# Kernel optimization log

Measured on AMD Instinct MI355X. Metric: run time of the kernel, lower is better.

## Reference

```python
import jax, jax.numpy as jnp
import numpy as np

EMB = 1024
DM = 64
NH = 16

def setup_inputs() -> dict:
    key = jax.random.key(0)
    ks = jax.random.split(key, 11)
    bs, slen = 2, 2048
    s = 1.0 / np.sqrt(EMB)
    inp = {
        'Q': jax.random.normal(ks[0], (bs, slen, EMB), jnp.float32),
        'K': jax.random.normal(ks[1], (bs, slen, EMB), jnp.float32),
        'V': jax.random.normal(ks[2], (bs, slen, EMB), jnp.float32),
        'Wq': jax.random.normal(ks[3], (EMB, DM * NH), jnp.float32) * s,
        'bq': jnp.zeros((DM * NH,), jnp.float32),
        'Wk': jax.random.normal(ks[4], (EMB, DM * NH), jnp.float32) * s,
        'bk': jnp.zeros((DM * NH,), jnp.float32),
        'Wv': jax.random.normal(ks[5], (EMB, DM * NH), jnp.float32) * s,
        'bv': jnp.zeros((DM * NH,), jnp.float32),
        'Wo': jax.random.normal(ks[6], (DM * NH, EMB), jnp.float32) * (1.0 / np.sqrt(DM * NH)),
        'bo': jnp.zeros((EMB,), jnp.float32),
    }
    return inp

def reference(Q, K, V, Wq, bq, Wk, bk, Wv, bv, Wo, bo):
    bs, q_len, _ = Q.shape
    kv_len = K.shape[1]
    scale = 1.0 / np.sqrt(DM)
    # project and split heads: (n, l, h, d)
    q = (scale * (Q @ Wq + bq)).reshape(bs, q_len, NH, DM)
    k = (K @ Wk + bk).reshape(bs, kv_len, NH, DM)
    v = (V @ Wv + bv).reshape(bs, kv_len, NH, DM)
    # scores (n, h, l, s) -- full S x S matrix, as in the original
    qk = jnp.einsum('nlhd,nshd->nhls', q, k)
    a = jax.nn.softmax(qk, axis=-1)  # dropout p=0 -> identity
    o = jnp.einsum('nhls,nshd->nlhd', a, v).reshape(bs, q_len, NH * DM)
    return o @ Wo + bo
```

## Files before the change

### kernel.cpp

```cpp
#include <hip/hip_runtime.h>
#include <cstdint>
#include <cstddef>

#define EMB  1024
#define DM   64
#define NH   16
#define SLEN 2048
#define BS   2

typedef _Float16 f16x8 __attribute__((ext_vector_type(8)));
typedef _Float16 f16x4 __attribute__((ext_vector_type(4)));
typedef __fp16   hf2   __attribute__((ext_vector_type(2)));
typedef __fp16   hf4   __attribute__((ext_vector_type(4)));
typedef __fp16   hf8   __attribute__((ext_vector_type(8)));
typedef float    f32x4 __attribute__((ext_vector_type(4)));

#define ASYNC_LD16(gp, lp)                                                        \
    __builtin_amdgcn_global_load_lds(                                             \
        (const __attribute__((address_space(1))) void*)(gp),                      \
        (__attribute__((address_space(3))) void*)(lp), 16, 0, 0)

__global__ __launch_bounds__(256)
void prep(const float* __restrict__ Q, const float* __restrict__ K,
          const float* __restrict__ V,
          const float* __restrict__ Wq, const float* __restrict__ Wk,
          const float* __restrict__ Wv, const float* __restrict__ Wo,
          _Float16* __restrict__ Qh, _Float16* __restrict__ Kh,
          _Float16* __restrict__ Vh,
          _Float16* __restrict__ WqT, _Float16* __restrict__ WkT,
          _Float16* __restrict__ WvT, _Float16* __restrict__ WoT)
{
    __shared__ float t[64][65];
    const int z = blockIdx.z;
    if (z < 3) {
        const float* in  = (z == 0) ? Q : (z == 1) ? K : V;
        _Float16*    out = (z == 0) ? Qh : (z == 1) ? Kh : Vh;
        size_t i = ((size_t)blockIdx.x * 256 + threadIdx.x) * 8;
        float4 a = *(const float4*)(in + i);
        float4 b = *(const float4*)(in + i + 4);
        f16x8 o;
        o[0] = (_Float16)a.x; o[1] = (_Float16)a.y; o[2] = (_Float16)a.z; o[3] = (_Float16)a.w;
        o[4] = (_Float16)b.x; o[5] = (_Float16)b.y; o[6] = (_Float16)b.z; o[7] = (_Float16)b.w;
        *(f16x8*)(out + i) = o;
        return;
    }
    if (blockIdx.x >= 256) return;
    const float* W;
    _Float16*    T;
    switch (z - 3) {
        case 0:  W = Wq; T = WqT; break;
        case 1:  W = Wk; T = WkT; break;
        case 2:  W = Wv; T = WvT; break;
        default: W = Wo; T = WoT; break;
    }
    const int tid = threadIdx.x;
    const int bn  = (blockIdx.x & 15) * 64;
    const int bk  = (blockIdx.x >> 4) * 64;

    #pragma unroll
    for (int p = 0; p < 4; ++p) {
        int row = p * 16 + (tid >> 4);
        int col = (tid & 15) * 4;
        float4 v = *(const float4*)(W + (size_t)(bk + row) * EMB + bn + col);
        t[row][col+0] = v.x; t[row][col+1] = v.y; t[row][col+2] = v.z; t[row][col+3] = v.w;
    }
    __syncthreads();
    #pragma unroll
    for (int p = 0; p < 4; ++p) {
        int nr = p * 16 + (tid >> 4);
        int kc = (tid & 15) * 4;
        f16x4 o;
        o[0] = (_Float16)t[kc+0][nr];
        o[1] = (_Float16)t[kc+1][nr];
        o[2] = (_Float16)t[kc+2][nr];
        o[3] = (_Float16)t[kc+3][nr];
        *(f16x4*)&T[(size_t)(bn + nr) * EMB + bk + kc] = o;
    }
}

__device__ __forceinline__
void gemm_core(const _Float16* __restrict__ A, const _Float16* __restrict__ Bt,
               const float* __restrict__ bias, float* __restrict__ Cf,
               _Float16* __restrict__ Ch, int M, int N, int K,
               float scale, int mode, int bx, int by)
{
    __shared__ __align__(16) _Float16 As[2][128 * 32];
    __shared__ __align__(16) _Float16 Bs[2][128 * 32];

    const int tid  = threadIdx.x;
    const int lane = tid & 63;
    const int wave = tid >> 6;
    const int c    = lane & 15;
    const int quad = lane >> 4;
    const int bm   = by * 128;
    const int bn   = bx * 128;
    const int wm   = (wave >> 1) * 64;
    const int wn   = (wave & 1) * 64;

    f32x4 acc[4][4];
    #pragma unroll
    for (int i = 0; i < 4; ++i)
        #pragma unroll
        for (int j = 0; j < 4; ++j)
            #pragma unroll
            for (int r = 0; r < 4; ++r) acc[i][j][r] = 0.f;

    const size_t Kb = (size_t)K * 2;
    const int    lc = ((tid & 3) ^ ((tid >> 4) & 3)) * 16;
    const char* gA = (const char*)A  + (size_t)(bm + (tid >> 2)) * Kb + lc;
    const char* gB = (const char*)Bt + (size_t)(bn + (tid >> 2)) * Kb + lc;

    const int NS = K / 32;

    auto stage = [&](int buf, int t) {
        const size_t ko = (size_t)t * 64;
        char* lA = (char*)&As[buf][0] + wave * 1024;
        char* lB = (char*)&Bs[buf][0] + wave * 1024;
        ASYNC_LD16(gA + ko,           lA);
        ASYNC_LD16(gA + 64*Kb + ko,   lA + 4096);
        ASYNC_LD16(gB + ko,           lB);
        ASYNC_LD16(gB + 64*Kb + ko,   lB + 4096);
    };

    stage(0, 0);
    __syncthreads();

    int cur = 0;
    for (int t = 0; t < NS; ++t) {
        if (t + 1 < NS) stage(cur ^ 1, t + 1);

        f16x8 af[4], bf[4];
        #pragma unroll
        for (int i = 0; i < 4; ++i)
            af[i] = *(const f16x8*)
                &As[cur][(wm + i*16 + c) * 32 + ((quad ^ ((c >> 2) & 3)) * 8)];
        #pragma unroll
        for (int j = 0; j < 4; ++j)
            bf[j] = *(const f16x8*)
                &Bs[cur][(wn + j*16 + c) * 32 + ((quad ^ ((c >> 2) & 3)) * 8)];
        #pragma unroll
        for (int i = 0; i < 4; ++i)
            #pragma unroll
            for (int j = 0; j < 4; ++j)
                acc[i][j] = __builtin_amdgcn_mfma_f32_16x16x32_f16(af[i], bf[j], acc[i][j], 0, 0, 0);

        __syncthreads();
        cur ^= 1;
    }

    float bcol[4];
    #pragma unroll
    for (int j = 0; j < 4; ++j) bcol[j] = bias[bn + wn + j * 16 + c];

    #pragma unroll
    for (int i = 0; i < 4; ++i) {
        int m0 = bm + wm + i * 16 + quad * 4;
        #pragma unroll
        for (int j = 0; j < 4; ++j) {
            int n = bn + wn + j * 16 + c;
            if (mode == 0) {
                #pragma unroll
                for (int r = 0; r < 4; ++r)
                    Cf[(size_t)(m0 + r) * N + n] = acc[i][j][r] + bcol[j];
            } else if (mode == 1) {
                int h = n >> 6, d = n & 63;
                #pragma unroll
                for (int r = 0; r < 4; ++r) {
                    int mm = m0 + r;
                    int b = mm >> 11, l = mm & (SLEN - 1);
                    Ch[(((size_t)(b * NH + h)) * SLEN + l) * DM + d] =
                        (_Float16)((acc[i][j][r] + bcol[j]) * scale);
                }
            } else {
                int h = n >> 6, d = n & 63;
                int b = m0 >> 11, l = m0 & (SLEN - 1);
                f16x4 o;
                #pragma unroll
                for (int r = 0; r < 4; ++r)
                    o[r] = (_Float16)(acc[i][j][r] + bcol[j]);
                *(f16x4*)&Ch[(((size_t)(b * NH + h)) * DM + d) * SLEN + l] = o;
            }
        }
    }
}

__device__ __forceinline__ void xcd_swz(int& bx, int& by)
{
    int wid = blockIdx.x + 8 * blockIdx.y;
    bx = wid >> 5;
    by = wid & 31;
}

__global__ __launch_bounds__(256)
void gemm_qkv(const _Float16* __restrict__ Qh, const _Float16* __restrict__ Kh,
              const _Float16* __restrict__ Vh,
              const _Float16* __restrict__ WqT, const _Float16* __restrict__ WkT,
              const _Float16* __restrict__ WvT,
              const float* __restrict__ bq, const float* __restrict__ bk,
              const float* __restrict__ bv,
              _Float16* __restrict__ q_ws, _Float16* __restrict__ k_ws,
              _Float16* __restrict__ v_ws)
{
    const _Float16 *A, *Bt;
    const float* bias;
    _Float16* Ch;
    float scale;
    int mode;
    if (blockIdx.z == 0)      { A = Qh; Bt = WqT; bias = bq; Ch = q_ws; scale = 0.18033688f; mode = 1; }
    else if (blockIdx.z == 1) { A = Kh; Bt = WkT; bias = bk; Ch = k_ws; scale = 1.0f;        mode = 1; }
    else                      { A = Vh; Bt = WvT; bias = bv; Ch = v_ws; scale = 1.0f;        mode = 2; }
    int bx, by; xcd_swz(bx, by);
    gemm_core(A, Bt, bias, nullptr, Ch, BS * SLEN, NH * DM, EMB, scale, mode, bx, by);
}

__global__ __launch_bounds__(256)
void gemm_out(const _Float16* __restrict__ Oh, const _Float16* __restrict__ WoT,
              const float* __restrict__ bo, float* __restrict__ out)
{
    int bx, by; xcd_swz(bx, by);
    gemm_core(Oh, WoT, bo, out, nullptr, BS * SLEN, EMB, NH * DM, 1.0f, 0, bx, by);
}

__global__ __launch_bounds__(512)
void attn_mfma(const _Float16* __restrict__ qw, const _Float16* __restrict__ kw,
               const _Float16* __restrict__ vwT, _Float16* __restrict__ ow)
{
    __shared__ __align__(16) _Float16 Kt[4][64 * 64];
    __shared__ __align__(16) _Float16 Vt[4][64 * 64];

    const int tid  = threadIdx.x;
    const int lane = tid & 63;
    const int wave = tid >> 6;
    const int c    = lane & 15;
    const int quad = lane >> 4;
    const int qg   = wave & 3;
    const int kh   = wave >> 2;
    const int bh   = blockIdx.y;
    const int b    = bh >> 4;
    const int h    = bh & 15;
    const int qbase = blockIdx.x * 128 + qg * 32;

    const _Float16* kb = kw  + (size_t)bh * SLEN * DM;
    const _Float16* vb = vwT + (size_t)bh * DM * SLEN;
    const _Float16* qb = qw  + (size_t)bh * SLEN * DM;

    f16x8 qf[2][2];
    #pragma unroll
    for (int t = 0; t < 2; ++t)
        #pragma unroll
        for (int ch = 0; ch < 2; ++ch)
            qf[t][ch] = *(const f16x8*)(qb + (size_t)(qbase + t*16 + c) * DM + ch*32 + quad*8);

    f32x4 oacc[2][4];
    f32x4 lacc[2];
    #pragma unroll
    for (int t = 0; t < 2; ++t) {
        #pragma unroll
        for (int dg = 0; dg < 4; ++dg)
            #pragma unroll
            for (int r = 0; r < 4; ++r) oacc[t][dg][r] = 0.f;
        #pragma unroll
        for (int r = 0; r < 4; ++r) lacc[t][r] = 0.f;
    }

    const f16x8 ones8 = {(_Float16)1.f, (_Float16)1.f, (_Float16)1.f, (_Float16)1.f,
                         (_Float16)1.f, (_Float16)1.f, (_Float16)1.f, (_Float16)1.f};
    const f32x4 zero4 = {0.f, 0.f, 0.f, 0.f};

    const int r0  = wave * 8 + (lane >> 3);
    const int lc0 = (((lane & 7) ^ ((lane >> 3) & 7)) * 16);
    const char* gk = (const char*)kb + r0 * 128 + lc0;
    const char* gv = (const char*)vb + (size_t)r0 * 4096 + lc0;

    auto stage = [&](int buf) {
        char* pk = (char*)&Kt[buf][0] + wave * 1024;
        char* pv = (char*)&Vt[buf][0] + wave * 1024;
        ASYNC_LD16(gk, pk);
        ASYNC_LD16(gv, pv);
        gk += 8192;
        gv += 128;
    };

    stage(0); stage(1); stage(2);
    asm volatile("s_waitcnt vmcnt(4)" ::: "memory");
    __builtin_amdgcn_s_barrier();
    asm volatile("" ::: "memory");

    const int NT = SLEN / 64;
    for (int t = 0; t < NT; ++t) {
        stage((t + 3) & 3);
        const int cb = t & 3;

        f16x8 kf[2][2];
        #pragma unroll
        for (int kg = 0; kg < 2; ++kg)
            #pragma unroll
            for (int ch = 0; ch < 2; ++ch)
                kf[kg][ch] = *(const f16x8*)
                    &Kt[cb][(kh*32 + kg*16 + c) * 64 + (((ch*4 + quad) ^ (c & 7)) * 8)];

        f32x4 s[2][2];
        #pragma unroll
        for (int t2 = 0; t2 < 2; ++t2)
            #pragma unroll
            for (int kg = 0; kg < 2; ++kg) {
                s[t2][kg] = __builtin_amdgcn_mfma_f32_16x16x32_f16(kf[kg][0], qf[t2][0], zero4,    0, 0, 0);
                s[t2][kg] = __builtin_amdgcn_mfma_f32_16x16x32_f16(kf[kg][1], qf[t2][1], s[t2][kg], 0, 0, 0);
            }

        f16x8 pf8[2];
        #pragma unroll
        for (int t2 = 0; t2 < 2; ++t2) {
            hf4 h4[2];
            #pragma unroll
            for (int u = 0; u < 2; ++u) {
                float p0 = __builtin_amdgcn_exp2f(s[t2][u][0]);
                float p1 = __builtin_amdgcn_exp2f(s[t2][u][1]);
                float p2 = __builtin_amdgcn_exp2f(s[t2][u][2]);
                float p3 = __builtin_amdgcn_exp2f(s[t2][u][3]);
                hf2 lo = __builtin_amdgcn_cvt_pkrtz(p0, p1);
                hf2 hi = __builtin_amdgcn_cvt_pkrtz(p2, p3);
                h4[u] = __builtin_shufflevector(lo, hi, 0, 1, 2, 3);
            }
            hf8 h8 = __builtin_shufflevector(h4[0], h4[1], 0, 1, 2, 3, 4, 5, 6, 7);
            pf8[t2] = __builtin_bit_cast(f16x8, h8);
        }

        #pragma unroll
        for (int t2 = 0; t2 < 2; ++t2)
            lacc[t2] = __builtin_amdgcn_mfma_f32_16x16x32_f16(pf8[t2], ones8, lacc[t2], 0, 0, 0);

        #pragma unroll
        for (int dg = 0; dg < 4; ++dg) {
            f16x4 vf[2];
            #pragma unroll
            for (int u = 0; u < 2; ++u)
                vf[u] = *(const f16x4*)
                    &Vt[cb][(dg*16 + c) * 64 +
                            (((kh*4 + 2*u + (quad >> 1)) ^ (c & 7)) * 8) + (quad & 1) * 4];
            f16x8 v8 = __builtin_shufflevector(vf[0], vf[1], 0, 1, 2, 3, 4, 5, 6, 7);
            #pragma unroll
            for (int t2 = 0; t2 < 2; ++t2)
                oacc[t2][dg] = __builtin_amdgcn_mfma_f32_16x16x32_f16(pf8[t2], v8, oacc[t2][dg], 0, 0, 0);
        }

        asm volatile("s_waitcnt vmcnt(4)" ::: "memory");
        __builtin_amdgcn_s_barrier();
        asm volatile("" ::: "memory");
    }

    __syncthreads();

    float* mb = (float*)&Kt[0][0];
    #pragma unroll
    for (int t = 0; t < 2; ++t) {
        if (kh == 1) {
            float* p = mb + ((qg * 64 + lane) * 20);
            *(f32x4*)(p +  0) = oacc[t][0];
            *(f32x4*)(p +  4) = oacc[t][1];
            *(f32x4*)(p +  8) = oacc[t][2];
            *(f32x4*)(p + 12) = oacc[t][3];
            *(f32x4*)(p + 16) = lacc[t];
        }
        __syncthreads();
        if (kh == 0) {
            const float* p = mb + ((qg * 64 + lane) * 20);
            f32x4 po[4], pl;
            po[0] = *(const f32x4*)(p +  0);
            po[1] = *(const f32x4*)(p +  4);
            po[2] = *(const f32x4*)(p +  8);
            po[3] = *(const f32x4*)(p + 12);
            pl    = *(const f32x4*)(p + 16);
            #pragma unroll
            for (int r = 0; r < 4; ++r) {
                float linv = 1.0f / (lacc[t][r] + pl[r]);
                int row = qbase + t*16 + quad*4 + r;
                #pragma unroll
                for (int dg = 0; dg < 4; ++dg)
                    ow[((size_t)b * SLEN + row) * EMB + h * DM + dg*16 + c] =
                        (_Float16)((oacc[t][dg][r] + po[dg][r]) * linv);
            }
        }
        __syncthreads();
    }
}

extern "C" void kernel_launch(void* const* d_in, const int* in_sizes, int n_in,
                              void* d_out, int out_size, void* d_ws, size_t ws_size,
                              hipStream_t stream)
{
    const float* Q  = (const float*)d_in[0];
    const float* K  = (const float*)d_in[1];
    const float* V  = (const float*)d_in[2];
    const float* Wq = (const float*)d_in[3];
    const float* bq = (const float*)d_in[4];
    const float* Wk = (const float*)d_in[5];
    const float* bk = (const float*)d_in[6];
    const float* Wv = (const float*)d_in[7];
    const float* bv = (const float*)d_in[8];
    const float* Wo = (const float*)d_in[9];
    const float* bo = (const float*)d_in[10];
    float* out = (float*)d_out;

    const size_t MN = (size_t)BS * SLEN * NH * DM;
    const size_t WW = (size_t)EMB * NH * DM;

    _Float16* base = (_Float16*)d_ws;
    _Float16* Qh   = base;
    _Float16* Kh   = Qh  + MN;
    _Float16* Vh   = Kh  + MN;
    _Float16* WqT  = Vh  + MN;
    _Float16* WkT  = WqT + WW;
    _Float16* WvT  = WkT + WW;
    _Float16* WoT  = WvT + WW;
    _Float16* q_ws = WoT + WW;
    _Float16* k_ws = q_ws + MN;
    _Float16* v_ws = k_ws + MN;
    _Float16* o_ws = v_ws + MN;

    dim3 blk(256);

    prep<<<dim3(2048, 1, 7), blk, 0, stream>>>(Q, K, V, Wq, Wk, Wv, Wo,
                                               Qh, Kh, Vh, WqT, WkT, WvT, WoT);

    gemm_qkv<<<dim3(8, 32, 3), blk, 0, stream>>>(Qh, Kh, Vh, WqT, WkT, WvT,
                                                 bq, bk, bv, q_ws, k_ws, v_ws);

    attn_mfma<<<dim3(SLEN / 128, BS * NH), dim3(512), 0, stream>>>(q_ws, k_ws, v_ws, o_ws);

    gemm_out<<<dim3(8, 32, 1), blk, 0, stream>>>(o_ws, WoT, bo, out);
}
```

Before: 229.6 us.

## Fuse fp32-to-fp16 activation conversion into QKV GEMM and retile GEMMs

Removes the separate pass that converts Q, K and V activations from fp32 to fp16. The QKV GEMM now loads fp32 A tiles through registers, converts them and writes them into swizzled LDS, while B still uses async global-to-LDS loads. GEMM tiles change from 128x128x32 to 64x128x64, doubling the grid. This saves a full read/write round trip of the activations, but the A path is now synchronous register loads and reads twice the bytes per element.

```diff
diff --git a/kernel.cpp b/kernel.cpp
--- a/kernel.cpp
+++ b/kernel.cpp
@@ -21,33 +21,15 @@
         (__attribute__((address_space(3))) void*)(lp), 16, 0, 0)
 
 __global__ __launch_bounds__(256)
-void prep(const float* __restrict__ Q, const float* __restrict__ K,
-          const float* __restrict__ V,
-          const float* __restrict__ Wq, const float* __restrict__ Wk,
+void prep(const float* __restrict__ Wq, const float* __restrict__ Wk,
           const float* __restrict__ Wv, const float* __restrict__ Wo,
-          _Float16* __restrict__ Qh, _Float16* __restrict__ Kh,
-          _Float16* __restrict__ Vh,
           _Float16* __restrict__ WqT, _Float16* __restrict__ WkT,
           _Float16* __restrict__ WvT, _Float16* __restrict__ WoT)
 {
     __shared__ float t[64][65];
-    const int z = blockIdx.z;
-    if (z < 3) {
-        const float* in  = (z == 0) ? Q : (z == 1) ? K : V;
-        _Float16*    out = (z == 0) ? Qh : (z == 1) ? Kh : Vh;
-        size_t i = ((size_t)blockIdx.x * 256 + threadIdx.x) * 8;
-        float4 a = *(const float4*)(in + i);
-        float4 b = *(const float4*)(in + i + 4);
-        f16x8 o;
-        o[0] = (_Float16)a.x; o[1] = (_Float16)a.y; o[2] = (_Float16)a.z; o[3] = (_Float16)a.w;
-        o[4] = (_Float16)b.x; o[5] = (_Float16)b.y; o[6] = (_Float16)b.z; o[7] = (_Float16)b.w;
-        *(f16x8*)(out + i) = o;
-        return;
-    }
-    if (blockIdx.x >= 256) return;
     const float* W;
     _Float16*    T;
-    switch (z - 3) {
+    switch (blockIdx.z) {
         case 0:  W = Wq; T = WqT; break;
         case 1:  W = Wk; T = WkT; break;
         case 2:  W = Wv; T = WvT; break;
@@ -78,72 +60,133 @@
     }
 }
 
+template <bool A32>
 __device__ __forceinline__
-void gemm_core(const _Float16* __restrict__ A, const _Float16* __restrict__ Bt,
+void gemm_core(const void* __restrict__ Aptr, const _Float16* __restrict__ Bt,
                const float* __restrict__ bias, float* __restrict__ Cf,
                _Float16* __restrict__ Ch, int M, int N, int K,
                float scale, int mode, int bx, int by)
 {
-    __shared__ __align__(16) _Float16 As[2][128 * 32];
-    __shared__ __align__(16) _Float16 Bs[2][128 * 32];
+    __shared__ __align__(16) _Float16 As[2][64 * 64];
+    __shared__ __align__(16) _Float16 Bs[2][128 * 64];
 
     const int tid  = threadIdx.x;
     const int lane = tid & 63;
     const int wave = tid >> 6;
     const int c    = lane & 15;
     const int quad = lane >> 4;
-    const int bm   = by * 128;
+    const int bm   = by * 64;
     const int bn   = bx * 128;
-    const int wm   = (wave >> 1) * 64;
+    const int wm   = (wave >> 1) * 32;
     const int wn   = (wave & 1) * 64;
 
-    f32x4 acc[4][4];
-    #pragma unroll
-    for (int i = 0; i < 4; ++i)
+    f32x4 acc[2][4];
+    #pragma unroll
+    for (int i = 0; i < 2; ++i)
         #pragma unroll
         for (int j = 0; j < 4; ++j)
             #pragma unroll
             for (int r = 0; r < 4; ++r) acc[i][j][r] = 0.f;
 
     const size_t Kb = (size_t)K * 2;
-    const int    lc = ((tid & 3) ^ ((tid >> 4) & 3)) * 16;
-    const char* gA = (const char*)A  + (size_t)(bm + (tid >> 2)) * Kb + lc;
-    const char* gB = (const char*)Bt + (size_t)(bn + (tid >> 2)) * Kb + lc;
-
-    const int NS = K / 32;
-
-    auto stage = [&](int buf, int t) {
-        const size_t ko = (size_t)t * 64;
+    const int    lc = ((tid & 7) ^ ((tid >> 3) & 7)) * 16;
+    const char* gB = (const char*)Bt + (size_t)(bn + (tid >> 3)) * Kb + lc;
+
+    const char*  gA16 = nullptr;
+    const float* gA32 = nullptr;
+    int aswz0 = 0, aswz1 = 0;
+    if constexpr (A32) {
+        const int ar  = tid >> 2;
+        const int acg = tid & 3;
+        gA32  = (const float*)Aptr + (size_t)(bm + ar) * K + acg * 16;
+        aswz0 = ar * 64 + (((2*acg    ) ^ (ar & 7)) * 8);
+        aswz1 = ar * 64 + (((2*acg + 1) ^ (ar & 7)) * 8);
+    } else {
+        gA16 = (const char*)Aptr + (size_t)(bm + (tid >> 3)) * Kb + lc;
+    }
+
+    const int NS = K / 64;
+
+    auto stageB = [&](int buf, int t) {
+        const size_t ko = (size_t)t * 128;
+        char* lB = (char*)&Bs[buf][0] + wave * 1024;
+        ASYNC_LD16(gB + ko,           lB);
+        ASYNC_LD16(gB + 32*Kb + ko,   lB + 4096);
+        ASYNC_LD16(gB + 64*Kb + ko,   lB + 8192);
+        ASYNC_LD16(gB + 96*Kb + ko,   lB + 12288);
+    };
+    auto stageA16 = [&](int buf, int t) {
+        const size_t ko = (size_t)t * 128;
         char* lA = (char*)&As[buf][0] + wave * 1024;
-        char* lB = (char*)&Bs[buf][0] + wave * 1024;
-        ASYNC_LD16(gA + ko,           lA);
-        ASYNC_LD16(gA + 64*Kb + ko,   lA + 4096);
-        ASYNC_LD16(gB + ko,           lB);
-        ASYNC_LD16(gB + 64*Kb + ko,   lB + 4096);
+        ASYNC_LD16(gA16 + ko,         lA);
+        ASYNC_LD16(gA16 + 32*Kb + ko, lA + 4096);
     };
-
-    stage(0, 0);
+    auto writeA32 = [&](int buf, const float4& a0, const float4& a1,
+                        const float4& a2, const float4& a3) {
+        f16x8 h0, h1;
+        h0[0] = (_Float16)a0.x; h0[1] = (_Float16)a0.y;
+        h0[2] = (_Float16)a0.z; h0[3] = (_Float16)a0.w;
+        h0[4] = (_Float16)a1.x; h0[5] = (_Float16)a1.y;
+        h0[6] = (_Float16)a1.z; h0[7] = (_Float16)a1.w;
+        h1[0] = (_Float16)a2.x; h1[1] = (_Float16)a2.y;
+        h1[2] = (_Float16)a2.z; h1[3] = (_Float16)a2.w;
+        h1[4] = (_Float16)a3.x; h1[5] = (_Float16)a3.y;
+        h1[6] = (_Float16)a3.z; h1[7] = (_Float16)a3.w;
+        *(f16x8*)&As[buf][aswz0] = h0;
+        *(f16x8*)&As[buf][aswz1] = h1;
+    };
+
+    if constexpr (A32) {
+        float4 a0 = *(const float4*)(gA32 + 0);
+        float4 a1 = *(const float4*)(gA32 + 4);
+        float4 a2 = *(const float4*)(gA32 + 8);
+        float4 a3 = *(const float4*)(gA32 + 12);
+        stageB(0, 0);
+        writeA32(0, a0, a1, a2, a3);
+    } else {
+        stageA16(0, 0);
+        stageB(0, 0);
+    }
     __syncthreads();
 
     int cur = 0;
     for (int t = 0; t < NS; ++t) {
-        if (t + 1 < NS) stage(cur ^ 1, t + 1);
-
-        f16x8 af[4], bf[4];
-        #pragma unroll
-        for (int i = 0; i < 4; ++i)
-            af[i] = *(const f16x8*)
-                &As[cur][(wm + i*16 + c) * 32 + ((quad ^ ((c >> 2) & 3)) * 8)];
-        #pragma unroll
-        for (int j = 0; j < 4; ++j)
-            bf[j] = *(const f16x8*)
-                &Bs[cur][(wn + j*16 + c) * 32 + ((quad ^ ((c >> 2) & 3)) * 8)];
-        #pragma unroll
-        for (int i = 0; i < 4; ++i)
+        float4 a0, a1, a2, a3;
+        if constexpr (A32) {
+            if (t + 1 < NS) {
+                const float* p = gA32 + (size_t)(t + 1) * 64;
+                a0 = *(const float4*)(p + 0);
+                a1 = *(const float4*)(p + 4);
+                a2 = *(const float4*)(p + 8);
+                a3 = *(const float4*)(p + 12);
+            }
+        }
+        if (t + 1 < NS) {
+            if constexpr (!A32) stageA16(cur ^ 1, t + 1);
+            stageB(cur ^ 1, t + 1);
+        }
+
+        #pragma unroll
+        for (int kk = 0; kk < 2; ++kk) {
+            f16x8 af[2], bf[4];
+            #pragma unroll
+            for (int i = 0; i < 2; ++i)
+                af[i] = *(const f16x8*)
+                    &As[cur][(wm + i*16 + c) * 64 + (((kk*4 + quad) ^ (c & 7)) * 8)];
             #pragma unroll
             for (int j = 0; j < 4; ++j)
-                acc[i][j] = __builtin_amdgcn_mfma_f32_16x16x32_f16(af[i], bf[j], acc[i][j], 0, 0, 0);
-
+                bf[j] = *(const f16x8*)
+                    &Bs[cur][(wn + j*16 + c) * 64 + (((kk*4 + quad) ^ (c & 7)) * 8)];
+            #pragma unroll
+            for (int i = 0; i < 2; ++i)
+                #pragma unroll
+                for (int j = 0; j < 4; ++j)
+                    acc[i][j] = __builtin_amdgcn_mfma_f32_16x16x32_f16(af[i], bf[j], acc[i][j], 0, 0, 0);
+        }
+
+        if constexpr (A32) {
+            if (t + 1 < NS) writeA32(cur ^ 1, a0, a1, a2, a3);
+        }
         __syncthreads();
         cur ^= 1;
     }
@@ -153,7 +196,7 @@
     for (int j = 0; j < 4; ++j) bcol[j] = bias[bn + wn + j * 16 + c];
 
     #pragma unroll
-    for (int i = 0; i < 4; ++i) {
+    for (int i = 0; i < 2; ++i) {
         int m0 = bm + wm + i * 16 + quad * 4;
         #pragma unroll
         for (int j = 0; j < 4; ++j) {
@@ -187,13 +230,13 @@
 __device__ __forceinline__ void xcd_swz(int& bx, int& by)
 {
     int wid = blockIdx.x + 8 * blockIdx.y;
-    bx = wid >> 5;
-    by = wid & 31;
+    bx = wid >> 6;
+    by = wid & 63;
 }
 
 __global__ __launch_bounds__(256)
-void gemm_qkv(const _Float16* __restrict__ Qh, const _Float16* __restrict__ Kh,
-              const _Float16* __restrict__ Vh,
+void gemm_qkv(const float* __restrict__ Q, const float* __restrict__ K,
+              const float* __restrict__ V,
               const _Float16* __restrict__ WqT, const _Float16* __restrict__ WkT,
               const _Float16* __restrict__ WvT,
               const float* __restrict__ bq, const float* __restrict__ bk,
@@ -201,16 +244,17 @@
               _Float16* __restrict__ q_ws, _Float16* __restrict__ k_ws,
               _Float16* __restrict__ v_ws)
 {
-    const _Float16 *A, *Bt;
+    const float* A;
+    const _Float16* Bt;
     const float* bias;
     _Float16* Ch;
     float scale;
     int mode;
-    if (blockIdx.z == 0)      { A = Qh; Bt = WqT; bias = bq; Ch = q_ws; scale = 0.18033688f; mode = 1; }
-    else if (blockIdx.z == 1) { A = Kh; Bt = WkT; bias = bk; Ch = k_ws; scale = 1.0f;        mode = 1; }
-    else                      { A = Vh; Bt = WvT; bias = bv; Ch = v_ws; scale = 1.0f;        mode = 2; }
+    if (blockIdx.z == 0)      { A = Q; Bt = WqT; bias = bq; Ch = q_ws; scale = 0.18033688f; mode = 1; }
+    else if (blockIdx.z == 1) { A = K; Bt = WkT; bias = bk; Ch = k_ws; scale = 1.0f;        mode = 1; }
+    else                      { A = V; Bt = WvT; bias = bv; Ch = v_ws; scale = 1.0f;        mode = 2; }
     int bx, by; xcd_swz(bx, by);
-    gemm_core(A, Bt, bias, nullptr, Ch, BS * SLEN, NH * DM, EMB, scale, mode, bx, by);
+    gemm_core<true>(A, Bt, bias, nullptr, Ch, BS * SLEN, NH * DM, EMB, scale, mode, bx, by);
 }
 
 __global__ __launch_bounds__(256)
@@ -218,7 +262,7 @@
               const float* __restrict__ bo, float* __restrict__ out)
 {
     int bx, by; xcd_swz(bx, by);
-    gemm_core(Oh, WoT, bo, out, nullptr, BS * SLEN, EMB, NH * DM, 1.0f, 0, bx, by);
+    gemm_core<false>(Oh, WoT, bo, out, nullptr, BS * SLEN, EMB, NH * DM, 1.0f, 0, bx, by);
 }
 
 __global__ __launch_bounds__(512)
@@ -304,7 +348,7 @@
         for (int t2 = 0; t2 < 2; ++t2)
             #pragma unroll
             for (int kg = 0; kg < 2; ++kg) {
-                s[t2][kg] = __builtin_amdgcn_mfma_f32_16x16x32_f16(kf[kg][0], qf[t2][0], zero4,    0, 0, 0);
+                s[t2][kg] = __builtin_amdgcn_mfma_f32_16x16x32_f16(kf[kg][0], qf[t2][0], zero4,     0, 0, 0);
                 s[t2][kg] = __builtin_amdgcn_mfma_f32_16x16x32_f16(kf[kg][1], qf[t2][1], s[t2][kg], 0, 0, 0);
             }
 
@@ -406,10 +450,7 @@
     const size_t WW = (size_t)EMB * NH * DM;
 
     _Float16* base = (_Float16*)d_ws;
-    _Float16* Qh   = base;
-    _Float16* Kh   = Qh  + MN;
-    _Float16* Vh   = Kh  + MN;
-    _Float16* WqT  = Vh  + MN;
+    _Float16* WqT  = base;
     _Float16* WkT  = WqT + WW;
     _Float16* WvT  = WkT + WW;
     _Float16* WoT  = WvT + WW;
@@ -420,13 +461,13 @@
 
     dim3 blk(256);
 
-    prep<<<dim3(2048, 1, 7), blk, 0, stream>>>(Q, K, V, Wq, Wk, Wv, Wo,
-                                               Qh, Kh, Vh, WqT, WkT, WvT, WoT);
-
-    gemm_qkv<<<dim3(8, 32, 3), blk, 0, stream>>>(Qh, Kh, Vh, WqT, WkT, WvT,
+    prep<<<dim3(256, 1, 4), blk, 0, stream>>>(Wq, Wk, Wv, Wo,
+                                              WqT, WkT, WvT, WoT);
+
+    gemm_qkv<<<dim3(8, 64, 3), blk, 0, stream>>>(Q, K, V, WqT, WkT, WvT,
                                                  bq, bk, bv, q_ws, k_ws, v_ws);
 
     attn_mfma<<<dim3(SLEN / 128, BS * NH), dim3(512), 0, stream>>>(q_ws, k_ws, v_ws, o_ws);
 
-    gemm_out<<<dim3(8, 32, 1), blk, 0, stream>>>(o_ws, WoT, bo, out);
-}
+    gemm_out<<<dim3(8, 64, 1), blk, 0, stream>>>(o_ws, WoT, bo, out);
+}
```

Measured after the change: 231.5 us. Within noise of the previous version (+0.8%).
